# Kernel optimization log

Measured on AMD Instinct MI355X. Metric: run time of the kernel, lower is better.

Reference implementation:

```python
import jax, jax.numpy as jnp
import numpy as np

R = 32       # voxel_resolution
GROUPS = 8   # GroupNorm groups
EPS = 1e-5


def setup_inputs() -> dict:
    key = jax.random.key(0)
    ks = jax.random.split(key, 8)
    B, N, Cin, Cout = 4, 16384, 64, 128
    coords = jax.random.uniform(ks[0], (B, N, 3), dtype=jnp.float32)
    features = jax.random.normal(ks[1], (B, Cin, N), dtype=jnp.float32) * 0.5
    s1 = 1.0 / np.sqrt(Cin * 27)
    s2 = 1.0 / np.sqrt(Cout * 27)
    sm = 1.0 / np.sqrt(Cin)
    return {
        "coords": coords,
        "features": features,
        "conv1_w": jax.random.normal(ks[2], (Cout, Cin, 3, 3, 3), dtype=jnp.float32) * s1,
        "conv1_b": jnp.zeros((Cout,), jnp.float32),
        "gn1_g": jnp.ones((Cout,), jnp.float32),
        "gn1_b": jnp.zeros((Cout,), jnp.float32),
        "conv2_w": jax.random.normal(ks[3], (Cout, Cout, 3, 3, 3), dtype=jnp.float32) * s2,
        "conv2_b": jnp.zeros((Cout,), jnp.float32),
        "gn2_g": jnp.ones((Cout,), jnp.float32),
        "gn2_b": jnp.zeros((Cout,), jnp.float32),
        "mlp_w": jax.random.normal(ks[4], (Cout, Cin), dtype=jnp.float32) * sm,
        "mlp_b": jnp.zeros((Cout,), jnp.float32),
        "gnp_g": jnp.ones((Cout,), jnp.float32),
        "gnp_b": jnp.zeros((Cout,), jnp.float32),
    }


def _group_norm(x, gamma, beta, axes):
    # x: [B, C, ...]; normalize within channel groups over `axes` of the
    # grouped view [B, G, C//G, ...]. axes=(2,) => per-location GN (matches
    # nn.GroupNorm applied to per-voxel feature rows [Nvox, C]).
    B, C = x.shape[0], x.shape[1]
    xr = x.reshape(B, GROUPS, C // GROUPS, *x.shape[2:])
    mu = xr.mean(axis=axes, keepdims=True)
    var = ((xr - mu) ** 2).mean(axis=axes, keepdims=True)
    xn = ((xr - mu) * jax.lax.rsqrt(var + EPS)).reshape(x.shape)
    shp = (1, C) + (1,) * (x.ndim - 2)
    return xn * gamma.reshape(shp) + beta.reshape(shp)


def _conv3(x, w, b):
    y = jax.lax.conv_general_dilated(
        x, w, (1, 1, 1), 'SAME',
        dimension_numbers=('NCDHW', 'OIDHW', 'NCDHW'))
    return y + b.reshape(1, -1, 1, 1, 1)


def reference(coords, features, conv1_w, conv1_b, gn1_g, gn1_b,
              conv2_w, conv2_b, gn2_g, gn2_b, mlp_w, mlp_b, gnp_g, gnp_b):
    B, Cin, N = features.shape
    Cout = conv1_w.shape[0]

    # ---- voxelize: average-scatter point features into [B,Cin,R,R,R] ----
    c = coords * R                               # voxel-unit coords in [0,R)
    lo = jnp.floor(c)
    idx = jnp.clip(lo.astype(jnp.int32), 0, R - 1)   # [B,N,3]
    bidx = jnp.arange(B, dtype=jnp.int32)[:, None]
    flat = ((bidx * R + idx[..., 0]) * R + idx[..., 1]) * R + idx[..., 2]
    seg = flat.reshape(-1)                       # [B*N]
    fT = features.transpose(0, 2, 1).reshape(B * N, Cin)
    sums = jax.ops.segment_sum(fT, seg, num_segments=B * R * R * R)
    cnt = jax.ops.segment_sum(jnp.ones((B * N,), fT.dtype), seg,
                              num_segments=B * R * R * R)
    grid = (sums / jnp.maximum(cnt, 1.0)[:, None]).reshape(
        B, R, R, R, Cin).transpose(0, 4, 1, 2, 3)

    # ---- voxel branch: conv -> GN -> SiLU -> (dropout=id) -> conv -> GN -> SiLU
    h = jax.nn.silu(_group_norm(_conv3(grid, conv1_w, conv1_b), gn1_g, gn1_b, (2,)))
    h = jax.nn.silu(_group_norm(_conv3(h, conv2_w, conv2_b), gn2_g, gn2_b, (2,)))

    # ---- trilinear devoxelize: gather-interpolate back to points ----
    frac = c - lo                                # [B,N,3]
    hi = jnp.clip(idx + 1, 0, R - 1)
    gridf = h.transpose(0, 2, 3, 4, 1).reshape(B, R * R * R, Cout)
    barange = jnp.arange(B)[:, None]
    out = jnp.zeros((B, N, Cout), h.dtype)
    for dx in (0, 1):
        wx = frac[..., 0] if dx else 1.0 - frac[..., 0]
        ix = hi[..., 0] if dx else idx[..., 0]
        for dy in (0, 1):
            wy = frac[..., 1] if dy else 1.0 - frac[..., 1]
            iy = hi[..., 1] if dy else idx[..., 1]
            for dz in (0, 1):
                wz = frac[..., 2] if dz else 1.0 - frac[..., 2]
                iz = hi[..., 2] if dz else idx[..., 2]
                fi = (ix * R + iy) * R + iz       # [B,N]
                vals = gridf[barange, fi]         # [B,N,Cout]
                out = out + (wx * wy * wz)[..., None] * vals
    vox_pts = out.transpose(0, 2, 1)              # [B,Cout,N]

    # ---- point branch: SharedMLP = 1x1 conv + GroupNorm + SiLU ----
    pf = jnp.einsum('oi,bin->bon', mlp_w, features) + mlp_b[None, :, None]
    pf = jax.nn.silu(_group_norm(pf, gnp_g, gnp_b, (2, 3)))

    return pf + vox_pts
```

## Files before the change

kernel.cpp:

```cpp
#include <hip/hip_runtime.h>

typedef unsigned short u16;
typedef __attribute__((ext_vector_type(8))) short s16x8;
typedef __attribute__((ext_vector_type(4))) float f32x4;

#define R3 32768
#define NPTS 16384

__device__ __forceinline__ float b2f(u16 u) {
  union { unsigned int i; float f; } v; v.i = ((unsigned int)u) << 16; return v.f;
}
__device__ __forceinline__ u16 f2b(float f) {
  union { float f; unsigned int i; } v; v.f = f;
  unsigned int x = v.i;
  return (u16)((x + 0x7fffu + ((x >> 16) & 1u)) >> 16);
}
__device__ __forceinline__ void split2(float x, u16& h, u16& l) {
  h = f2b(x); l = f2b(x - b2f(h));
}
__device__ __forceinline__ float silu(float x) {
  return x / (1.f + __expf(-x));
}

__global__ void convert_weights(const float* __restrict__ w1, const float* __restrict__ w2,
                                const float* __restrict__ wm,
                                u16* __restrict__ Wh1, u16* __restrict__ Wl1,
                                u16* __restrict__ Wh2, u16* __restrict__ Wl2,
                                u16* __restrict__ Whm, u16* __restrict__ Wlm) {
  int e = blockIdx.x * 256 + threadIdx.x;
  if (e < 27 * 128 * 64) {
    int t = e / (128 * 64), co = (e / 64) % 128, ci = e % 64;
    split2(w1[(co * 64 + ci) * 27 + t], Wh1[e], Wl1[e]);
  }
  if (e < 27 * 128 * 128) {
    int t = e / (128 * 128), co = (e / 128) % 128, ci = e % 128;
    split2(w2[(co * 128 + ci) * 27 + t], Wh2[e], Wl2[e]);
  }
  if (e < 128 * 64) split2(wm[e], Whm[e], Wlm[e]);
}

__global__ void calc_pvox(const float* __restrict__ coords, int* __restrict__ pvox) {
  int t = blockIdx.x * 256 + threadIdx.x;
  if (t >= 4 * NPTS) return;
  const float* cp = coords + (size_t)t * 3;
  int ix = min(max((int)floorf(cp[0] * 32.f), 0), 31);
  int iy = min(max((int)floorf(cp[1] * 32.f), 0), 31);
  int iz = min(max((int)floorf(cp[2] * 32.f), 0), 31);
  pvox[t] = (ix * 32 + iy) * 32 + iz;
}

__global__ void __launch_bounds__(256)
scatter_feats(const float* __restrict__ features, const int* __restrict__ pvox,
              float* __restrict__ Gsum, float* __restrict__ Gcnt) {
  __shared__ float trans[64][65];
  __shared__ int vox[64];
  const int tid = threadIdx.x;
  const int bi = blockIdx.x >> 8;
  const int n0 = (blockIdx.x & 255) << 6;
  if (tid < 64) vox[tid] = pvox[bi * NPTS + n0 + tid];
  for (int e = tid; e < 4096; e += 256) {
    int ci = e >> 6, nn = e & 63;
    trans[nn][ci] = features[((size_t)bi * 64 + ci) * NPTS + n0 + nn];
  }
  __syncthreads();
  const int wave = tid >> 6, lane = tid & 63;
  for (int pi = 0; pi < 16; ++pi) {
    int nn = wave * 16 + pi;
    int v = vox[nn];
    atomicAdd(&Gsum[((size_t)bi * R3 + v) * 64 + lane], trans[nn][lane]);
    if (lane == 0) atomicAdd(&Gcnt[bi * R3 + v], 1.f);
  }
}

__global__ void __launch_bounds__(256)
finalize_grid(const float* __restrict__ Gsum, const float* __restrict__ Gcnt,
              u16* __restrict__ X1) {
  size_t g = (size_t)blockIdx.x * 256 + threadIdx.x;
  float c = fmaxf(Gcnt[g >> 4], 1.f);
  float4 s = ((const float4*)Gsum)[g];
  unsigned h0 = f2b(s.x / c), h1 = f2b(s.y / c), h2 = f2b(s.z / c), h3 = f2b(s.w / c);
  uint2 o; o.x = h0 | (h1 << 16); o.y = h2 | (h3 << 16);
  *(uint2*)(X1 + g * 4) = o;
}

template<int CIN>
__global__ void __launch_bounds__(256)
conv_mfma16(const u16* __restrict__ X, const u16* __restrict__ Wh, const u16* __restrict__ Wl,
            const float* __restrict__ bias, const float* __restrict__ gamma,
            const float* __restrict__ beta, u16* __restrict__ Yb) {
  constexpr int CINP = CIN + 8;
  constexpr int ROWS = 136;
  constexpr int KS = CIN / 32;
  constexpr int XBYTES = ROWS * CINP * 2;
  constexpr int SBYTES = 4 * 2 * 32 * 33 * 4;
  __shared__ __align__(16) char ldsbuf[(XBYTES > SBYTES) ? XBYTES : SBYTES];
  u16* Xs = (u16*)ldsbuf;
  float* ldsW = (float*)ldsbuf;

  const int tid = threadIdx.x;
  const int wave = tid >> 6, lane = tid & 63;
  const int l15 = lane & 15, q = lane >> 4;
  const int cobase = wave * 32;

  const int bi = blockIdx.x >> 8;
  const int rem = blockIdx.x & 255;
  const int x = rem >> 3, y0 = (rem & 7) << 2;

  u16 oneb = f2b(1.0f), lidb = f2b((float)(l15 + 1));
  s16x8 vone, vlid;
#pragma unroll
  for (int e = 0; e < 8; ++e) { vone[e] = (short)oneb; vlid[e] = (short)lidb; }
  f32x4 z4 = {0.f, 0.f, 0.f, 0.f};
  f32x4 d1 = __builtin_amdgcn_mfma_f32_16x16x32_bf16(vlid, vone, z4, 0, 0, 0);
  f32x4 d2 = __builtin_amdgcn_mfma_f32_16x16x32_bf16(vone, vlid, z4, 0, 0, 0);
  int mdec[4], ndec[4];
#pragma unroll
  for (int r = 0; r < 4; ++r) {
    mdec[r] = (int)(d1[r] * 0.03125f + 0.5f) - 1;
    ndec[r] = (int)(d2[r] * 0.03125f + 0.5f) - 1;
  }

  f32x4 acc[2][2][4];
#pragma unroll
  for (int a = 0; a < 2; ++a)
#pragma unroll
    for (int b = 0; b < 2; ++b)
#pragma unroll
      for (int c = 0; c < 4; ++c) acc[a][b][c] = (f32x4){0.f, 0.f, 0.f, 0.f};

  constexpr int CH8 = CIN / 8;
  for (int g = 0; g < 9; ++g) {
    __syncthreads();
    const int dx = g / 3 - 1, dy = g % 3 - 1;
    const int xs = x + dx;
    for (int c = tid; c < ROWS * CH8; c += 256) {
      int rr = c / CH8, k = (c % CH8) * 8;
      uint4 val; val.x = val.y = val.z = val.w = 0u;
      int vy = rr / 34;
      int zz = rr - vy * 34 - 1;
      int ys = y0 + vy + dy;
      if (xs >= 0 && xs < 32 && ys >= 0 && ys < 32 && zz >= 0 && zz < 32)
        val = *(const uint4*)(X + ((size_t)bi * R3 + (size_t)((xs * 32 + ys) * 32 + zz)) * CIN + k);
      *(uint4*)(&Xs[rr * CINP + k]) = val;
    }
    __syncthreads();
    for (int dz = 0; dz < 3; ++dz) {
      const int t = g * 3 + dz;
#pragma unroll
      for (int kb = 0; kb < KS; ++kb) {
        const int ko = kb * 32 + q * 8;
        s16x8 ah[2], al[2], bb[2][4];
#pragma unroll
        for (int ct = 0; ct < 2; ++ct) {
          size_t wo = ((size_t)(t * 128 + cobase + ct * 16 + l15)) * CIN + ko;
          ah[ct] = *(const s16x8*)(Wh + wo);
          al[ct] = *(const s16x8*)(Wl + wo);
        }
#pragma unroll
        for (int vt = 0; vt < 2; ++vt)
#pragma unroll
          for (int ln = 0; ln < 4; ++ln)
            bb[vt][ln] = *(const s16x8*)(&Xs[(ln * 34 + vt * 16 + l15 + dz) * CINP + ko]);
#pragma unroll
        for (int ct = 0; ct < 2; ++ct)
#pragma unroll
          for (int vt = 0; vt < 2; ++vt)
#pragma unroll
            for (int ln = 0; ln < 4; ++ln) {
              acc[ct][vt][ln] = __builtin_amdgcn_mfma_f32_16x16x32_bf16(
                  ah[ct], bb[vt][ln], acc[ct][vt][ln], 0, 0, 0);
              acc[ct][vt][ln] = __builtin_amdgcn_mfma_f32_16x16x32_bf16(
                  al[ct], bb[vt][ln], acc[ct][vt][ln], 0, 0, 0);
            }
      }
    }
  }

  const int half = lane >> 5, zl = lane & 31;
  for (int p = 0; p < 2; ++p) {
    __syncthreads();
#pragma unroll
    for (int l2 = 0; l2 < 2; ++l2)
#pragma unroll
      for (int ct = 0; ct < 2; ++ct)
#pragma unroll
        for (int vt = 0; vt < 2; ++vt)
#pragma unroll
          for (int r = 0; r < 4; ++r)
            ldsW[((wave * 2 + l2) * 32 + ct * 16 + mdec[r]) * 33 + vt * 16 + ndec[r]] =
                acc[ct][vt][2 * p + l2][r];
    __syncthreads();
    const int co0 = cobase + half * 16;
#pragma unroll
    for (int l2 = 0; l2 < 2; ++l2) {
      float v[16];
#pragma unroll
      for (int j = 0; j < 16; ++j)
        v[j] = ldsW[((wave * 2 + l2) * 32 + half * 16 + j) * 33 + zl] + bias[co0 + j];
      float mu = 0.f;
#pragma unroll
      for (int j = 0; j < 16; ++j) mu += v[j];
      mu *= 0.0625f;
      float var = 0.f;
#pragma unroll
      for (int j = 0; j < 16; ++j) { float d = v[j] - mu; var = fmaf(d, d, var); }
      var *= 0.0625f;
      float rs = rsqrtf(var + 1e-5f);
#pragma unroll
      for (int j = 0; j < 16; ++j) {
        float xn = (v[j] - mu) * rs * gamma[co0 + j] + beta[co0 + j];
        v[j] = silu(xn);
      }
      size_t row = (size_t)bi * R3 + (size_t)((x * 32 + y0 + 2 * p + l2) * 32 + zl);
      u16 outv[16];
#pragma unroll
      for (int j = 0; j < 16; ++j) outv[j] = f2b(v[j]);
      u16* yp = Yb + row * 128 + co0;
      *(uint4*)(yp)     = *(uint4*)(outv);
      *(uint4*)(yp + 8) = *(uint4*)(outv + 8);
    }
  }
}

__global__ void __launch_bounds__(256)
mlp_mfma(const float* __restrict__ features, const u16* __restrict__ Whm,
         const u16* __restrict__ Wlm, const float* __restrict__ mb,
         u16* __restrict__ pf, float* __restrict__ stats) {
  constexpr int XBYTES = 64 * 72 * 2;
  constexpr int SBYTES = 4 * 64 * 33 * 4;
  __shared__ __align__(16) char ldsbuf[(XBYTES > SBYTES) ? XBYTES : SBYTES];
  u16* Xs = (u16*)ldsbuf;
  float* ldsW = (float*)ldsbuf;

  const int tid = threadIdx.x;
  const int wave = tid >> 6, lane = tid & 63;
  const int l15 = lane & 15, q = lane >> 4;
  const int cobase = wave * 32;
  const int bi = blockIdx.x >> 8;
  const int n0 = (blockIdx.x & 255) << 6;

  u16 oneb = f2b(1.0f), lidb = f2b((float)(l15 + 1));
  s16x8 vone, vlid;
#pragma unroll
  for (int e = 0; e < 8; ++e) { vone[e] = (short)oneb; vlid[e] = (short)lidb; }
  f32x4 z4 = {0.f, 0.f, 0.f, 0.f};
  f32x4 d1 = __builtin_amdgcn_mfma_f32_16x16x32_bf16(vlid, vone, z4, 0, 0, 0);
  f32x4 d2 = __builtin_amdgcn_mfma_f32_16x16x32_bf16(vone, vlid, z4, 0, 0, 0);
  int mdec[4], ndec[4];
#pragma unroll
  for (int r = 0; r < 4; ++r) {
    mdec[r] = (int)(d1[r] * 0.03125f + 0.5f) - 1;
    ndec[r] = (int)(d2[r] * 0.03125f + 0.5f) - 1;
  }

  for (int e = tid; e < 4096; e += 256) {
    int ci = e >> 6, nn = e & 63;
    Xs[nn * 72 + ci] = f2b(features[((size_t)bi * 64 + ci) * NPTS + n0 + nn]);
  }
  __syncthreads();

  f32x4 acc[2][4];
#pragma unroll
  for (int a = 0; a < 2; ++a)
#pragma unroll
    for (int b = 0; b < 4; ++b) acc[a][b] = (f32x4){0.f, 0.f, 0.f, 0.f};

#pragma unroll
  for (int kb = 0; kb < 2; ++kb) {
    const int ko = kb * 32 + q * 8;
    s16x8 ah[2], al[2], bb[4];
#pragma unroll
    for (int ct = 0; ct < 2; ++ct) {
      size_t wo = ((size_t)(cobase + ct * 16 + l15)) * 64 + ko;
      ah[ct] = *(const s16x8*)(Whm + wo);
      al[ct] = *(const s16x8*)(Wlm + wo);
    }
#pragma unroll
    for (int vt = 0; vt < 4; ++vt)
      bb[vt] = *(const s16x8*)(&Xs[(vt * 16 + l15) * 72 + ko]);
#pragma unroll
    for (int ct = 0; ct < 2; ++ct)
#pragma unroll
      for (int vt = 0; vt < 4; ++vt) {
        acc[ct][vt] = __builtin_amdgcn_mfma_f32_16x16x32_bf16(ah[ct], bb[vt], acc[ct][vt], 0, 0, 0);
        acc[ct][vt] = __builtin_amdgcn_mfma_f32_16x16x32_bf16(al[ct], bb[vt], acc[ct][vt], 0, 0, 0);
      }
  }

  __syncthreads();
#pragma unroll
  for (int ct = 0; ct < 2; ++ct)
#pragma unroll
    for (int vt = 0; vt < 4; ++vt)
#pragma unroll
      for (int r = 0; r < 4; ++r)
        ldsW[(wave * 64 + vt * 16 + ndec[r]) * 33 + ct * 16 + mdec[r]] = acc[ct][vt][r];
  __syncthreads();

  float v[32];
  float s0 = 0.f, q0 = 0.f, s1 = 0.f, q1 = 0.f;
#pragma unroll
  for (int j = 0; j < 32; ++j) {
    v[j] = ldsW[(wave * 64 + lane) * 33 + j] + mb[cobase + j];
    if (j < 16) { s0 += v[j]; q0 = fmaf(v[j], v[j], q0); }
    else        { s1 += v[j]; q1 = fmaf(v[j], v[j], q1); }
  }
  u16 outv[32];
#pragma unroll
  for (int j = 0; j < 32; ++j) outv[j] = f2b(v[j]);
  u16* yp = pf + ((size_t)bi * NPTS + n0 + lane) * 128 + cobase;
#pragma unroll
  for (int k = 0; k < 4; ++k) *(uint4*)(yp + 8 * k) = *(uint4*)(outv + 8 * k);

#pragma unroll
  for (int off = 32; off > 0; off >>= 1) {
    s0 += __shfl_xor(s0, off); q0 += __shfl_xor(q0, off);
    s1 += __shfl_xor(s1, off); q1 += __shfl_xor(q1, off);
  }
  if (lane == 0) {
    atomicAdd(&stats[(bi * 8 + 2 * wave + 0) * 2 + 0], s0);
    atomicAdd(&stats[(bi * 8 + 2 * wave + 0) * 2 + 1], q0);
    atomicAdd(&stats[(bi * 8 + 2 * wave + 1) * 2 + 0], s1);
    atomicAdd(&stats[(bi * 8 + 2 * wave + 1) * 2 + 1], q1);
  }
}

__global__ void __launch_bounds__(256)
final_fuse(const float* __restrict__ coords, const u16* __restrict__ H,
           const u16* __restrict__ pf, const float* __restrict__ stats,
           const float* __restrict__ gg, const float* __restrict__ gb,
           float* __restrict__ out) {
  __shared__ float trans[64][130];
  const int tid = threadIdx.x;
  const int wave = tid >> 6, lane = tid & 63;
  const int bi = blockIdx.x >> 8;
  const int p0 = (blockIdx.x & 255) << 6;
  const int co = lane * 2;
  const int grp = co >> 4;
  const float cntInv = 1.f / (16.f * 16384.f);
  float S  = stats[(bi * 8 + grp) * 2 + 0];
  float SS = stats[(bi * 8 + grp) * 2 + 1];
  float mu = S * cntInv;
  float var = SS * cntInv - mu * mu;
  float rs = rsqrtf(var + 1e-5f);
  float g0 = gg[co], g1 = gg[co + 1], b0 = gb[co], b1 = gb[co + 1];

  for (int pi = 0; pi < 16; ++pi) {
    int pl = wave * 16 + pi;
    int p = p0 + pl;
    const float* cp = coords + ((size_t)bi * NPTS + p) * 3;
    float cx = cp[0] * 32.f, cy = cp[1] * 32.f, cz = cp[2] * 32.f;
    float fx = floorf(cx), fy = floorf(cy), fz = floorf(cz);
    int ix = min(max((int)fx, 0), 31);
    int iy = min(max((int)fy, 0), 31);
    int iz = min(max((int)fz, 0), 31);
    float rx = cx - fx, ry = cy - fy, rz = cz - fz;
    int hx = min(ix + 1, 31), hy = min(iy + 1, 31), hz = min(iz + 1, 31);
    float a0 = 0.f, a1 = 0.f;
#pragma unroll
    for (int k = 0; k < 8; ++k) {
      int xb = k >> 2, yb = (k >> 1) & 1, zb = k & 1;
      float w = (xb ? rx : 1.f - rx) * (yb ? ry : 1.f - ry) * (zb ? rz : 1.f - rz);
      int vi = ((xb ? hx : ix) * 32 + (yb ? hy : iy)) * 32 + (zb ? hz : iz);
      unsigned hv = *(const unsigned*)(H + ((size_t)bi * R3 + vi) * 128 + co);
      a0 += w * b2f((u16)(hv & 0xffff));
      a1 += w * b2f((u16)(hv >> 16));
    }
    unsigned pv = *(const unsigned*)(pf + ((size_t)bi * NPTS + p) * 128 + co);
    float q0 = (b2f((u16)(pv & 0xffff)) - mu) * rs * g0 + b0;
    float q1 = (b2f((u16)(pv >> 16)) - mu) * rs * g1 + b1;
    trans[pl][co]     = silu(q0) + a0;
    trans[pl][co + 1] = silu(q1) + a1;
  }
  __syncthreads();
  for (int e = tid; e < 8192; e += 256) {
    int c = e >> 6, pp = e & 63;
    out[((size_t)bi * 128 + c) * NPTS + p0 + pp] = trans[pp][c];
  }
}

extern "C" void kernel_launch(void* const* d_in, const int* in_sizes, int n_in,
                              void* d_out, int out_size, void* d_ws, size_t ws_size,
                              hipStream_t stream) {
  const float* coords   = (const float*)d_in[0];
  const float* features = (const float*)d_in[1];
  const float* conv1_w  = (const float*)d_in[2];
  const float* conv1_b  = (const float*)d_in[3];
  const float* gn1_g    = (const float*)d_in[4];
  const float* gn1_b    = (const float*)d_in[5];
  const float* conv2_w  = (const float*)d_in[6];
  const float* conv2_b  = (const float*)d_in[7];
  const float* gn2_g    = (const float*)d_in[8];
  const float* gn2_b    = (const float*)d_in[9];
  const float* mlp_w    = (const float*)d_in[10];
  const float* mlp_b    = (const float*)d_in[11];
  const float* gnp_g    = (const float*)d_in[12];
  const float* gnp_b    = (const float*)d_in[13];

  char* ws = (char*)d_ws;
  float* Gsum = (float*)(ws + 0);
  u16*   H    = (u16*)(ws + 0);
  u16*   X1   = (u16*)(ws + 33554432);
  u16*   X2   = (u16*)(ws + 50331648);
  float* Gcnt = (float*)(ws + 83886080);
  float* stats = (float*)(ws + 84410368);
  int*   pvox = (int*)(ws + 84414464);
  u16*   pf   = (u16*)(ws + 84676608);
  u16*   Wh1  = (u16*)(ws + 101453824);
  u16*   Wl1  = (u16*)(ws + 101896192);
  u16*   Wh2  = (u16*)(ws + 102338560);
  u16*   Wl2  = (u16*)(ws + 103223296);
  u16*   Whm  = (u16*)(ws + 104108032);
  u16*   Wlm  = (u16*)(ws + 104124416);

  hipMemsetAsync(ws, 0, 33554432, stream);
  hipMemsetAsync(ws + 83886080, 0, 524288 + 4096, stream);

  convert_weights<<<(27 * 128 * 128 + 255) / 256, 256, 0, stream>>>(
      conv1_w, conv2_w, mlp_w, Wh1, Wl1, Wh2, Wl2, Whm, Wlm);
  calc_pvox<<<(4 * NPTS + 255) / 256, 256, 0, stream>>>(coords, pvox);
  scatter_feats<<<1024, 256, 0, stream>>>(features, pvox, Gsum, Gcnt);
  finalize_grid<<<8192, 256, 0, stream>>>(Gsum, Gcnt, X1);
  conv_mfma16<64><<<1024, 256, 0, stream>>>(
      X1, Wh1, Wl1, conv1_b, gn1_g, gn1_b, X2);
  mlp_mfma<<<1024, 256, 0, stream>>>(features, Whm, Wlm, mlp_b, pf, stats);
  conv_mfma16<128><<<1024, 256, 0, stream>>>(
      X2, Wh2, Wl2, conv2_b, gn2_g, gn2_b, H);
  final_fuse<<<1024, 256, 0, stream>>>(coords, H, pf, stats, gnp_g, gnp_b,
                                       (float*)d_out);
}
```

Baseline: 647.5 us.

## Split conv output channels across two blocks with XCD-aware tile mapping

Each conv block now computes 64 output channels instead of 128, with each wave doing a single 16-channel tile. This doubles the grid to 2048 blocks and cuts accumulator registers, and launch bounds now ask for 4 blocks per SM. Block IDs are remapped so the tiles on each XCD share spatial neighbourhoods, which should improve L2 reuse. The cost is that every input halo tile is loaded into LDS twice, once per channel half, so global and LDS load traffic per MFMA goes up.

```diff
diff --git a/kernel.cpp b/kernel.cpp
--- a/kernel.cpp
+++ b/kernel.cpp
@@ -84,15 +84,16 @@
 }
 
 template<int CIN>
-__global__ void __launch_bounds__(256)
-conv_mfma16(const u16* __restrict__ X, const u16* __restrict__ Wh, const u16* __restrict__ Wl,
-            const float* __restrict__ bias, const float* __restrict__ gamma,
-            const float* __restrict__ beta, u16* __restrict__ Yb) {
+__global__ void __launch_bounds__(256, 4)
+conv_mfma16c(const u16* __restrict__ X, const u16* __restrict__ Wh, const u16* __restrict__ Wl,
+             const float* __restrict__ bias, const float* __restrict__ gamma,
+             const float* __restrict__ beta, u16* __restrict__ Yb) {
   constexpr int CINP = CIN + 8;
   constexpr int ROWS = 136;
   constexpr int KS = CIN / 32;
+  constexpr int CH8 = CIN / 8;
   constexpr int XBYTES = ROWS * CINP * 2;
-  constexpr int SBYTES = 4 * 2 * 32 * 33 * 4;
+  constexpr int SBYTES = 4 * 2 * 16 * 33 * 4;
   __shared__ __align__(16) char ldsbuf[(XBYTES > SBYTES) ? XBYTES : SBYTES];
   u16* Xs = (u16*)ldsbuf;
   float* ldsW = (float*)ldsbuf;
@@ -100,11 +101,15 @@
   const int tid = threadIdx.x;
   const int wave = tid >> 6, lane = tid & 63;
   const int l15 = lane & 15, q = lane >> 4;
-  const int cobase = wave * 32;
-
-  const int bi = blockIdx.x >> 8;
-  const int rem = blockIdx.x & 255;
+
+  const int bid = blockIdx.x;
+  const int xcd = bid & 7, jj = bid >> 3;
+  const int coblk = jj >> 7;
+  const int tile = xcd * 128 + (jj & 127);
+  const int bi = tile >> 8;
+  const int rem = tile & 255;
   const int x = rem >> 3, y0 = (rem & 7) << 2;
+  const int co0 = coblk * 64 + wave * 16;
 
   u16 oneb = f2b(1.0f), lidb = f2b((float)(l15 + 1));
   s16x8 vone, vlid;
@@ -120,15 +125,12 @@
     ndec[r] = (int)(d2[r] * 0.03125f + 0.5f) - 1;
   }
 
-  f32x4 acc[2][2][4];
-#pragma unroll
-  for (int a = 0; a < 2; ++a)
-#pragma unroll
-    for (int b = 0; b < 2; ++b)
-#pragma unroll
-      for (int c = 0; c < 4; ++c) acc[a][b][c] = (f32x4){0.f, 0.f, 0.f, 0.f};
-
-  constexpr int CH8 = CIN / 8;
+  f32x4 acc[2][4];
+#pragma unroll
+  for (int b = 0; b < 2; ++b)
+#pragma unroll
+    for (int c = 0; c < 4; ++c) acc[b][c] = (f32x4){0.f, 0.f, 0.f, 0.f};
+
   for (int g = 0; g < 9; ++g) {
     __syncthreads();
     const int dx = g / 3 - 1, dy = g % 3 - 1;
@@ -149,12 +151,11 @@
 #pragma unroll
       for (int kb = 0; kb < KS; ++kb) {
         const int ko = kb * 32 + q * 8;
-        s16x8 ah[2], al[2], bb[2][4];
-#pragma unroll
-        for (int ct = 0; ct < 2; ++ct) {
-          size_t wo = ((size_t)(t * 128 + cobase + ct * 16 + l15)) * CIN + ko;
-          ah[ct] = *(const s16x8*)(Wh + wo);
-          al[ct] = *(const s16x8*)(Wl + wo);
+        s16x8 ah, al, bb[2][4];
+        {
+          size_t wo = ((size_t)(t * 128 + co0 + l15)) * CIN + ko;
+          ah = *(const s16x8*)(Wh + wo);
+          al = *(const s16x8*)(Wl + wo);
         }
 #pragma unroll
         for (int vt = 0; vt < 2; ++vt)
@@ -162,16 +163,14 @@
           for (int ln = 0; ln < 4; ++ln)
             bb[vt][ln] = *(const s16x8*)(&Xs[(ln * 34 + vt * 16 + l15 + dz) * CINP + ko]);
 #pragma unroll
-        for (int ct = 0; ct < 2; ++ct)
-#pragma unroll
-          for (int vt = 0; vt < 2; ++vt)
-#pragma unroll
-            for (int ln = 0; ln < 4; ++ln) {
-              acc[ct][vt][ln] = __builtin_amdgcn_mfma_f32_16x16x32_bf16(
-                  ah[ct], bb[vt][ln], acc[ct][vt][ln], 0, 0, 0);
-              acc[ct][vt][ln] = __builtin_amdgcn_mfma_f32_16x16x32_bf16(
-                  al[ct], bb[vt][ln], acc[ct][vt][ln], 0, 0, 0);
-            }
+        for (int vt = 0; vt < 2; ++vt)
+#pragma unroll
+          for (int ln = 0; ln < 4; ++ln) {
+            acc[vt][ln] = __builtin_amdgcn_mfma_f32_16x16x32_bf16(
+                ah, bb[vt][ln], acc[vt][ln], 0, 0, 0);
+            acc[vt][ln] = __builtin_amdgcn_mfma_f32_16x16x32_bf16(
+                al, bb[vt][ln], acc[vt][ln], 0, 0, 0);
+          }
       }
     }
   }
@@ -182,43 +181,37 @@
 #pragma unroll
     for (int l2 = 0; l2 < 2; ++l2)
 #pragma unroll
-      for (int ct = 0; ct < 2; ++ct)
-#pragma unroll
-        for (int vt = 0; vt < 2; ++vt)
-#pragma unroll
-          for (int r = 0; r < 4; ++r)
-            ldsW[((wave * 2 + l2) * 32 + ct * 16 + mdec[r]) * 33 + vt * 16 + ndec[r]] =
-                acc[ct][vt][2 * p + l2][r];
+      for (int vt = 0; vt < 2; ++vt)
+#pragma unroll
+        for (int r = 0; r < 4; ++r)
+          ldsW[((wave * 2 + l2) * 16 + mdec[r]) * 33 + vt * 16 + ndec[r]] =
+              acc[vt][2 * p + l2][r];
     __syncthreads();
-    const int co0 = cobase + half * 16;
-#pragma unroll
-    for (int l2 = 0; l2 < 2; ++l2) {
-      float v[16];
-#pragma unroll
-      for (int j = 0; j < 16; ++j)
-        v[j] = ldsW[((wave * 2 + l2) * 32 + half * 16 + j) * 33 + zl] + bias[co0 + j];
-      float mu = 0.f;
-#pragma unroll
-      for (int j = 0; j < 16; ++j) mu += v[j];
-      mu *= 0.0625f;
-      float var = 0.f;
-#pragma unroll
-      for (int j = 0; j < 16; ++j) { float d = v[j] - mu; var = fmaf(d, d, var); }
-      var *= 0.0625f;
-      float rs = rsqrtf(var + 1e-5f);
-#pragma unroll
-      for (int j = 0; j < 16; ++j) {
-        float xn = (v[j] - mu) * rs * gamma[co0 + j] + beta[co0 + j];
-        v[j] = silu(xn);
-      }
-      size_t row = (size_t)bi * R3 + (size_t)((x * 32 + y0 + 2 * p + l2) * 32 + zl);
-      u16 outv[16];
-#pragma unroll
-      for (int j = 0; j < 16; ++j) outv[j] = f2b(v[j]);
-      u16* yp = Yb + row * 128 + co0;
-      *(uint4*)(yp)     = *(uint4*)(outv);
-      *(uint4*)(yp + 8) = *(uint4*)(outv + 8);
+    float v[16];
+#pragma unroll
+    for (int j = 0; j < 16; ++j)
+      v[j] = ldsW[((wave * 2 + half) * 16 + j) * 33 + zl] + bias[co0 + j];
+    float mu = 0.f;
+#pragma unroll
+    for (int j = 0; j < 16; ++j) mu += v[j];
+    mu *= 0.0625f;
+    float var = 0.f;
+#pragma unroll
+    for (int j = 0; j < 16; ++j) { float d = v[j] - mu; var = fmaf(d, d, var); }
+    var *= 0.0625f;
+    float rs = rsqrtf(var + 1e-5f);
+#pragma unroll
+    for (int j = 0; j < 16; ++j) {
+      float xn = (v[j] - mu) * rs * gamma[co0 + j] + beta[co0 + j];
+      v[j] = silu(xn);
     }
+    size_t row = (size_t)bi * R3 + (size_t)((x * 32 + y0 + 2 * p + half) * 32 + zl);
+    u16 outv[16];
+#pragma unroll
+    for (int j = 0; j < 16; ++j) outv[j] = f2b(v[j]);
+    u16* yp = Yb + row * 128 + co0;
+    *(uint4*)(yp)     = *(uint4*)(outv);
+    *(uint4*)(yp + 8) = *(uint4*)(outv + 8);
   }
 }
 
@@ -421,10 +414,10 @@
   calc_pvox<<<(4 * NPTS + 255) / 256, 256, 0, stream>>>(coords, pvox);
   scatter_feats<<<1024, 256, 0, stream>>>(features, pvox, Gsum, Gcnt);
   finalize_grid<<<8192, 256, 0, stream>>>(Gsum, Gcnt, X1);
-  conv_mfma16<64><<<1024, 256, 0, stream>>>(
+  conv_mfma16c<64><<<2048, 256, 0, stream>>>(
       X1, Wh1, Wl1, conv1_b, gn1_g, gn1_b, X2);
   mlp_mfma<<<1024, 256, 0, stream>>>(features, Whm, Wlm, mlp_b, pf, stats);
-  conv_mfma16<128><<<1024, 256, 0, stream>>>(
+  conv_mfma16c<128><<<2048, 256, 0, stream>>>(
       X2, Wh2, Wl2, conv2_b, gn2_g, gn2_b, H);
   final_fuse<<<1024, 256, 0, stream>>>(coords, H, pf, stats, gnp_g, gnp_b,
                                        (float*)d_out);
```

After: 664.7 us. +2.6%, slower.

## Re-split conv waves over channels and y-lines; fuse voxel index into scatter

Applied to the files above, without the earlier changes.

The conv kernel now assigns each wave 64 output channels and 2 y-lines instead of 32 channels and 4 lines. This trades fewer LDS activation loads per wave for more global weight loads. The GroupNorm/SiLU epilogue is reorganised so each thread handles 32 channels of one voxel. The separate voxel-index kernel is folded into the scatter kernel to remove a launch and a buffer round trip.

```diff
diff --git a/kernel.cpp b/kernel.cpp
--- a/kernel.cpp
+++ b/kernel.cpp
@@ -39,25 +39,21 @@
   if (e < 128 * 64) split2(wm[e], Whm[e], Wlm[e]);
 }
 
-__global__ void calc_pvox(const float* __restrict__ coords, int* __restrict__ pvox) {
-  int t = blockIdx.x * 256 + threadIdx.x;
-  if (t >= 4 * NPTS) return;
-  const float* cp = coords + (size_t)t * 3;
-  int ix = min(max((int)floorf(cp[0] * 32.f), 0), 31);
-  int iy = min(max((int)floorf(cp[1] * 32.f), 0), 31);
-  int iz = min(max((int)floorf(cp[2] * 32.f), 0), 31);
-  pvox[t] = (ix * 32 + iy) * 32 + iz;
-}
-
 __global__ void __launch_bounds__(256)
-scatter_feats(const float* __restrict__ features, const int* __restrict__ pvox,
+scatter_feats(const float* __restrict__ coords, const float* __restrict__ features,
               float* __restrict__ Gsum, float* __restrict__ Gcnt) {
   __shared__ float trans[64][65];
   __shared__ int vox[64];
   const int tid = threadIdx.x;
   const int bi = blockIdx.x >> 8;
   const int n0 = (blockIdx.x & 255) << 6;
-  if (tid < 64) vox[tid] = pvox[bi * NPTS + n0 + tid];
+  if (tid < 64) {
+    const float* cp = coords + ((size_t)bi * NPTS + n0 + tid) * 3;
+    int ix = min(max((int)floorf(cp[0] * 32.f), 0), 31);
+    int iy = min(max((int)floorf(cp[1] * 32.f), 0), 31);
+    int iz = min(max((int)floorf(cp[2] * 32.f), 0), 31);
+    vox[tid] = (ix * 32 + iy) * 32 + iz;
+  }
   for (int e = tid; e < 4096; e += 256) {
     int ci = e >> 6, nn = e & 63;
     trans[nn][ci] = features[((size_t)bi * 64 + ci) * NPTS + n0 + nn];
@@ -85,14 +81,15 @@
 
 template<int CIN>
 __global__ void __launch_bounds__(256)
-conv_mfma16(const u16* __restrict__ X, const u16* __restrict__ Wh, const u16* __restrict__ Wl,
-            const float* __restrict__ bias, const float* __restrict__ gamma,
-            const float* __restrict__ beta, u16* __restrict__ Yb) {
+conv_mfma_c4(const u16* __restrict__ X, const u16* __restrict__ Wh, const u16* __restrict__ Wl,
+             const float* __restrict__ bias, const float* __restrict__ gamma,
+             const float* __restrict__ beta, u16* __restrict__ Yb) {
   constexpr int CINP = CIN + 8;
   constexpr int ROWS = 136;
   constexpr int KS = CIN / 32;
+  constexpr int CH8 = CIN / 8;
   constexpr int XBYTES = ROWS * CINP * 2;
-  constexpr int SBYTES = 4 * 2 * 32 * 33 * 4;
+  constexpr int SBYTES = 2 * 128 * 33 * 4;
   __shared__ __align__(16) char ldsbuf[(XBYTES > SBYTES) ? XBYTES : SBYTES];
   u16* Xs = (u16*)ldsbuf;
   float* ldsW = (float*)ldsbuf;
@@ -100,7 +97,8 @@
   const int tid = threadIdx.x;
   const int wave = tid >> 6, lane = tid & 63;
   const int l15 = lane & 15, q = lane >> 4;
-  const int cobase = wave * 32;
+  const int cohalf = wave & 1, yhalf = wave >> 1;
+  const int co0 = cohalf * 64;
 
   const int bi = blockIdx.x >> 8;
   const int rem = blockIdx.x & 255;
@@ -120,15 +118,14 @@
     ndec[r] = (int)(d2[r] * 0.03125f + 0.5f) - 1;
   }
 
-  f32x4 acc[2][2][4];
-#pragma unroll
-  for (int a = 0; a < 2; ++a)
+  f32x4 acc[4][2][2];
+#pragma unroll
+  for (int a = 0; a < 4; ++a)
 #pragma unroll
     for (int b = 0; b < 2; ++b)
 #pragma unroll
-      for (int c = 0; c < 4; ++c) acc[a][b][c] = (f32x4){0.f, 0.f, 0.f, 0.f};
-
-  constexpr int CH8 = CIN / 8;
+      for (int c = 0; c < 2; ++c) acc[a][b][c] = (f32x4){0.f, 0.f, 0.f, 0.f};
+
   for (int g = 0; g < 9; ++g) {
     __syncthreads();
     const int dx = g / 3 - 1, dy = g % 3 - 1;
@@ -149,76 +146,77 @@
 #pragma unroll
       for (int kb = 0; kb < KS; ++kb) {
         const int ko = kb * 32 + q * 8;
-        s16x8 ah[2], al[2], bb[2][4];
-#pragma unroll
-        for (int ct = 0; ct < 2; ++ct) {
-          size_t wo = ((size_t)(t * 128 + cobase + ct * 16 + l15)) * CIN + ko;
+        s16x8 ah[4], al[4], bb[2][2];
+#pragma unroll
+        for (int ct = 0; ct < 4; ++ct) {
+          size_t wo = ((size_t)(t * 128 + co0 + ct * 16 + l15)) * CIN + ko;
           ah[ct] = *(const s16x8*)(Wh + wo);
           al[ct] = *(const s16x8*)(Wl + wo);
         }
 #pragma unroll
-        for (int vt = 0; vt < 2; ++vt)
-#pragma unroll
-          for (int ln = 0; ln < 4; ++ln)
-            bb[vt][ln] = *(const s16x8*)(&Xs[(ln * 34 + vt * 16 + l15 + dz) * CINP + ko]);
-#pragma unroll
-        for (int ct = 0; ct < 2; ++ct)
+        for (int l2 = 0; l2 < 2; ++l2)
 #pragma unroll
           for (int vt = 0; vt < 2; ++vt)
-#pragma unroll
-            for (int ln = 0; ln < 4; ++ln) {
-              acc[ct][vt][ln] = __builtin_amdgcn_mfma_f32_16x16x32_bf16(
-                  ah[ct], bb[vt][ln], acc[ct][vt][ln], 0, 0, 0);
-              acc[ct][vt][ln] = __builtin_amdgcn_mfma_f32_16x16x32_bf16(
-                  al[ct], bb[vt][ln], acc[ct][vt][ln], 0, 0, 0);
+            bb[l2][vt] = *(const s16x8*)(
+                &Xs[((yhalf * 2 + l2) * 34 + vt * 16 + l15 + dz) * CINP + ko]);
+#pragma unroll
+        for (int ct = 0; ct < 4; ++ct)
+#pragma unroll
+          for (int vt = 0; vt < 2; ++vt)
+#pragma unroll
+            for (int l2 = 0; l2 < 2; ++l2) {
+              acc[ct][vt][l2] = __builtin_amdgcn_mfma_f32_16x16x32_bf16(
+                  ah[ct], bb[l2][vt], acc[ct][vt][l2], 0, 0, 0);
+              acc[ct][vt][l2] = __builtin_amdgcn_mfma_f32_16x16x32_bf16(
+                  al[ct], bb[l2][vt], acc[ct][vt][l2], 0, 0, 0);
             }
       }
     }
   }
 
-  const int half = lane >> 5, zl = lane & 31;
   for (int p = 0; p < 2; ++p) {
     __syncthreads();
 #pragma unroll
-    for (int l2 = 0; l2 < 2; ++l2)
-#pragma unroll
-      for (int ct = 0; ct < 2; ++ct)
-#pragma unroll
-        for (int vt = 0; vt < 2; ++vt)
-#pragma unroll
-          for (int r = 0; r < 4; ++r)
-            ldsW[((wave * 2 + l2) * 32 + ct * 16 + mdec[r]) * 33 + vt * 16 + ndec[r]] =
-                acc[ct][vt][2 * p + l2][r];
+    for (int ct = 0; ct < 4; ++ct)
+#pragma unroll
+      for (int vt = 0; vt < 2; ++vt)
+#pragma unroll
+        for (int r = 0; r < 4; ++r) {
+          int co = co0 + ct * 16 + mdec[r];
+          int z  = vt * 16 + ndec[r];
+          ldsW[(yhalf * 128 + co) * 33 + z] = acc[ct][vt][p][r];
+        }
     __syncthreads();
-    const int co0 = cobase + half * 16;
-#pragma unroll
-    for (int l2 = 0; l2 < 2; ++l2) {
-      float v[16];
-#pragma unroll
-      for (int j = 0; j < 16; ++j)
-        v[j] = ldsW[((wave * 2 + l2) * 32 + half * 16 + j) * 33 + zl] + bias[co0 + j];
-      float mu = 0.f;
-#pragma unroll
-      for (int j = 0; j < 16; ++j) mu += v[j];
-      mu *= 0.0625f;
-      float var = 0.f;
-#pragma unroll
-      for (int j = 0; j < 16; ++j) { float d = v[j] - mu; var = fmaf(d, d, var); }
-      var *= 0.0625f;
-      float rs = rsqrtf(var + 1e-5f);
-#pragma unroll
-      for (int j = 0; j < 16; ++j) {
-        float xn = (v[j] - mu) * rs * gamma[co0 + j] + beta[co0 + j];
-        v[j] = silu(xn);
-      }
-      size_t row = (size_t)bi * R3 + (size_t)((x * 32 + y0 + 2 * p + l2) * 32 + zl);
-      u16 outv[16];
-#pragma unroll
-      for (int j = 0; j < 16; ++j) outv[j] = f2b(v[j]);
-      u16* yp = Yb + row * 128 + co0;
-      *(uint4*)(yp)     = *(uint4*)(outv);
-      *(uint4*)(yp + 8) = *(uint4*)(outv + 8);
-    }
+    const int vx = tid >> 2, quarter = tid & 3;
+    const int lsel = vx >> 5, z = vx & 31;
+    const int cq = quarter * 32;
+    float v[32];
+#pragma unroll
+    for (int j = 0; j < 32; ++j)
+      v[j] = ldsW[(lsel * 128 + cq + j) * 33 + z] + bias[cq + j];
+    float mu0 = 0.f, mu1 = 0.f;
+#pragma unroll
+    for (int j = 0; j < 16; ++j) { mu0 += v[j]; mu1 += v[16 + j]; }
+    mu0 *= 0.0625f; mu1 *= 0.0625f;
+    float va0 = 0.f, va1 = 0.f;
+#pragma unroll
+    for (int j = 0; j < 16; ++j) {
+      float d0 = v[j] - mu0;      va0 = fmaf(d0, d0, va0);
+      float d1v = v[16 + j] - mu1; va1 = fmaf(d1v, d1v, va1);
+    }
+    float rs0 = rsqrtf(va0 * 0.0625f + 1e-5f);
+    float rs1 = rsqrtf(va1 * 0.0625f + 1e-5f);
+    u16 outv[32];
+#pragma unroll
+    for (int j = 0; j < 32; ++j) {
+      float mu = (j < 16) ? mu0 : mu1, rs = (j < 16) ? rs0 : rs1;
+      float xn = (v[j] - mu) * rs * gamma[cq + j] + beta[cq + j];
+      outv[j] = f2b(silu(xn));
+    }
+    size_t row = (size_t)bi * R3 + (size_t)((x * 32 + y0 + lsel * 2 + p) * 32 + z);
+    u16* yp = Yb + row * 128 + cq;
+#pragma unroll
+    for (int k = 0; k < 4; ++k) *(uint4*)(yp + 8 * k) = *(uint4*)(outv + 8 * k);
   }
 }
 
@@ -404,7 +402,6 @@
   u16*   X2   = (u16*)(ws + 50331648);
   float* Gcnt = (float*)(ws + 83886080);
   float* stats = (float*)(ws + 84410368);
-  int*   pvox = (int*)(ws + 84414464);
   u16*   pf   = (u16*)(ws + 84676608);
   u16*   Wh1  = (u16*)(ws + 101453824);
   u16*   Wl1  = (u16*)(ws + 101896192);
@@ -418,13 +415,12 @@
 
   convert_weights<<<(27 * 128 * 128 + 255) / 256, 256, 0, stream>>>(
       conv1_w, conv2_w, mlp_w, Wh1, Wl1, Wh2, Wl2, Whm, Wlm);
-  calc_pvox<<<(4 * NPTS + 255) / 256, 256, 0, stream>>>(coords, pvox);
-  scatter_feats<<<1024, 256, 0, stream>>>(features, pvox, Gsum, Gcnt);
+  scatter_feats<<<1024, 256, 0, stream>>>(coords, features, Gsum, Gcnt);
   finalize_grid<<<8192, 256, 0, stream>>>(Gsum, Gcnt, X1);
-  conv_mfma16<64><<<1024, 256, 0, stream>>>(
+  conv_mfma_c4<64><<<1024, 256, 0, stream>>>(
       X1, Wh1, Wl1, conv1_b, gn1_g, gn1_b, X2);
   mlp_mfma<<<1024, 256, 0, stream>>>(features, Whm, Wlm, mlp_b, pf, stats);
-  conv_mfma16<128><<<1024, 256, 0, stream>>>(
+  conv_mfma_c4<128><<<1024, 256, 0, stream>>>(
       X2, Wh2, Wl2, conv2_b, gn2_g, gn2_b, H);
   final_fuse<<<1024, 256, 0, stream>>>(coords, H, pf, stats, gnp_g, gnp_b,
                                        (float*)d_out);
```

Measured after the change: 945.4 us. +46.0%, slower.

## Stage 6-row y halo per x-slice in conv and fuse voxel index into scatter

Applied to the files above, without the earlier changes.

The conv kernels now load one LDS tile per x offset, holding six y rows (ROWS 204) with the z halo, and reuse it across all three dy and three dz taps. Before, a fresh four-row tile was loaded for each of nine (dx,dy) pairs, so this cuts global loads and block barriers from nine to three per block. The cost is more LDS per block (about 55 KB for CIN=128), which may lower occupancy. The separate calc_pvox kernel is also removed and its voxel index computation is folded into scatter_feats, saving one launch and an intermediate buffer.

```diff
diff --git a/kernel.cpp b/kernel.cpp
--- a/kernel.cpp
+++ b/kernel.cpp
@@ -39,25 +39,21 @@
   if (e < 128 * 64) split2(wm[e], Whm[e], Wlm[e]);
 }
 
-__global__ void calc_pvox(const float* __restrict__ coords, int* __restrict__ pvox) {
-  int t = blockIdx.x * 256 + threadIdx.x;
-  if (t >= 4 * NPTS) return;
-  const float* cp = coords + (size_t)t * 3;
-  int ix = min(max((int)floorf(cp[0] * 32.f), 0), 31);
-  int iy = min(max((int)floorf(cp[1] * 32.f), 0), 31);
-  int iz = min(max((int)floorf(cp[2] * 32.f), 0), 31);
-  pvox[t] = (ix * 32 + iy) * 32 + iz;
-}
-
 __global__ void __launch_bounds__(256)
-scatter_feats(const float* __restrict__ features, const int* __restrict__ pvox,
+scatter_feats(const float* __restrict__ coords, const float* __restrict__ features,
               float* __restrict__ Gsum, float* __restrict__ Gcnt) {
   __shared__ float trans[64][65];
   __shared__ int vox[64];
   const int tid = threadIdx.x;
   const int bi = blockIdx.x >> 8;
   const int n0 = (blockIdx.x & 255) << 6;
-  if (tid < 64) vox[tid] = pvox[bi * NPTS + n0 + tid];
+  if (tid < 64) {
+    const float* cp = coords + ((size_t)bi * NPTS + n0 + tid) * 3;
+    int ix = min(max((int)floorf(cp[0] * 32.f), 0), 31);
+    int iy = min(max((int)floorf(cp[1] * 32.f), 0), 31);
+    int iz = min(max((int)floorf(cp[2] * 32.f), 0), 31);
+    vox[tid] = (ix * 32 + iy) * 32 + iz;
+  }
   for (int e = tid; e < 4096; e += 256) {
     int ci = e >> 6, nn = e & 63;
     trans[nn][ci] = features[((size_t)bi * 64 + ci) * NPTS + n0 + nn];
@@ -85,12 +81,14 @@
 
 template<int CIN>
 __global__ void __launch_bounds__(256)
-conv_mfma16(const u16* __restrict__ X, const u16* __restrict__ Wh, const u16* __restrict__ Wl,
-            const float* __restrict__ bias, const float* __restrict__ gamma,
-            const float* __restrict__ beta, u16* __restrict__ Yb) {
+conv_mfma_s3(const u16* __restrict__ X, const u16* __restrict__ Wh, const u16* __restrict__ Wl,
+             const float* __restrict__ bias, const float* __restrict__ gamma,
+             const float* __restrict__ beta, u16* __restrict__ Yb) {
   constexpr int CINP = CIN + 8;
-  constexpr int ROWS = 136;
+  constexpr int ROWS = 204;
+  constexpr int CH8 = CIN / 8;
   constexpr int KS = CIN / 32;
+  constexpr int NCH = ROWS * CH8;
   constexpr int XBYTES = ROWS * CINP * 2;
   constexpr int SBYTES = 4 * 2 * 32 * 33 * 4;
   __shared__ __align__(16) char ldsbuf[(XBYTES > SBYTES) ? XBYTES : SBYTES];
@@ -128,50 +126,54 @@
 #pragma unroll
       for (int c = 0; c < 4; ++c) acc[a][b][c] = (f32x4){0.f, 0.f, 0.f, 0.f};
 
-  constexpr int CH8 = CIN / 8;
-  for (int g = 0; g < 9; ++g) {
+  for (int dxs = 0; dxs < 3; ++dxs) {
     __syncthreads();
-    const int dx = g / 3 - 1, dy = g % 3 - 1;
-    const int xs = x + dx;
-    for (int c = tid; c < ROWS * CH8; c += 256) {
+    const int xs = x + dxs - 1;
+    for (int c = tid; c < NCH; c += 256) {
       int rr = c / CH8, k = (c % CH8) * 8;
       uint4 val; val.x = val.y = val.z = val.w = 0u;
-      int vy = rr / 34;
-      int zz = rr - vy * 34 - 1;
-      int ys = y0 + vy + dy;
+      int jy = rr / 34;
+      int pz = rr - jy * 34;
+      int ys = y0 + jy - 1, zz = pz - 1;
       if (xs >= 0 && xs < 32 && ys >= 0 && ys < 32 && zz >= 0 && zz < 32)
         val = *(const uint4*)(X + ((size_t)bi * R3 + (size_t)((xs * 32 + ys) * 32 + zz)) * CIN + k);
       *(uint4*)(&Xs[rr * CINP + k]) = val;
     }
     __syncthreads();
-    for (int dz = 0; dz < 3; ++dz) {
-      const int t = g * 3 + dz;
-#pragma unroll
-      for (int kb = 0; kb < KS; ++kb) {
-        const int ko = kb * 32 + q * 8;
-        s16x8 ah[2], al[2], bb[2][4];
-#pragma unroll
-        for (int ct = 0; ct < 2; ++ct) {
-          size_t wo = ((size_t)(t * 128 + cobase + ct * 16 + l15)) * CIN + ko;
-          ah[ct] = *(const s16x8*)(Wh + wo);
-          al[ct] = *(const s16x8*)(Wl + wo);
+    for (int dy = 0; dy < 3; ++dy) {
+      const int tb = dxs * 9 + dy * 3;
+      const int rbase = dy * 34;
+#pragma unroll
+      for (int dz = 0; dz < 3; ++dz) {
+        const int t = tb + dz;
+#pragma unroll
+        for (int kb = 0; kb < KS; ++kb) {
+          const int ko = kb * 32 + q * 8;
+          s16x8 ah[2], al[2], bb[2][4];
+#pragma unroll
+          for (int ct = 0; ct < 2; ++ct) {
+            size_t wo = ((size_t)(t * 128 + cobase + ct * 16 + l15)) * CIN + ko;
+            ah[ct] = *(const s16x8*)(Wh + wo);
+            al[ct] = *(const s16x8*)(Wl + wo);
+          }
+#pragma unroll
+          for (int vt = 0; vt < 2; ++vt)
+#pragma unroll
+            for (int ln = 0; ln < 4; ++ln)
+              bb[vt][ln] = *(const s16x8*)(
+                  &Xs[(rbase + ln * 34 + vt * 16 + l15 + dz) * CINP + ko]);
+#pragma unroll
+          for (int ct = 0; ct < 2; ++ct)
+#pragma unroll
+            for (int vt = 0; vt < 2; ++vt)
+#pragma unroll
+              for (int ln = 0; ln < 4; ++ln) {
+                acc[ct][vt][ln] = __builtin_amdgcn_mfma_f32_16x16x32_bf16(
+                    ah[ct], bb[vt][ln], acc[ct][vt][ln], 0, 0, 0);
+                acc[ct][vt][ln] = __builtin_amdgcn_mfma_f32_16x16x32_bf16(
+                    al[ct], bb[vt][ln], acc[ct][vt][ln], 0, 0, 0);
+              }
         }
-#pragma unroll
-        for (int vt = 0; vt < 2; ++vt)
-#pragma unroll
-          for (int ln = 0; ln < 4; ++ln)
-            bb[vt][ln] = *(const s16x8*)(&Xs[(ln * 34 + vt * 16 + l15 + dz) * CINP + ko]);
-#pragma unroll
-        for (int ct = 0; ct < 2; ++ct)
-#pragma unroll
-          for (int vt = 0; vt < 2; ++vt)
-#pragma unroll
-            for (int ln = 0; ln < 4; ++ln) {
-              acc[ct][vt][ln] = __builtin_amdgcn_mfma_f32_16x16x32_bf16(
-                  ah[ct], bb[vt][ln], acc[ct][vt][ln], 0, 0, 0);
-              acc[ct][vt][ln] = __builtin_amdgcn_mfma_f32_16x16x32_bf16(
-                  al[ct], bb[vt][ln], acc[ct][vt][ln], 0, 0, 0);
-            }
       }
     }
   }
@@ -404,7 +406,6 @@
   u16*   X2   = (u16*)(ws + 50331648);
   float* Gcnt = (float*)(ws + 83886080);
   float* stats = (float*)(ws + 84410368);
-  int*   pvox = (int*)(ws + 84414464);
   u16*   pf   = (u16*)(ws + 84676608);
   u16*   Wh1  = (u16*)(ws + 101453824);
   u16*   Wl1  = (u16*)(ws + 101896192);
@@ -418,13 +419,12 @@
 
   convert_weights<<<(27 * 128 * 128 + 255) / 256, 256, 0, stream>>>(
       conv1_w, conv2_w, mlp_w, Wh1, Wl1, Wh2, Wl2, Whm, Wlm);
-  calc_pvox<<<(4 * NPTS + 255) / 256, 256, 0, stream>>>(coords, pvox);
-  scatter_feats<<<1024, 256, 0, stream>>>(features, pvox, Gsum, Gcnt);
+  scatter_feats<<<1024, 256, 0, stream>>>(coords, features, Gsum, Gcnt);
   finalize_grid<<<8192, 256, 0, stream>>>(Gsum, Gcnt, X1);
-  conv_mfma16<64><<<1024, 256, 0, stream>>>(
+  conv_mfma_s3<64><<<1024, 256, 0, stream>>>(
       X1, Wh1, Wl1, conv1_b, gn1_g, gn1_b, X2);
   mlp_mfma<<<1024, 256, 0, stream>>>(features, Whm, Wlm, mlp_b, pf, stats);
-  conv_mfma16<128><<<1024, 256, 0, stream>>>(
+  conv_mfma_s3<128><<<1024, 256, 0, stream>>>(
       X2, Wh2, Wl2, conv2_b, gn2_g, gn2_b, H);
   final_fuse<<<1024, 256, 0, stream>>>(coords, H, pf, stats, gnp_g, gnp_b,
                                        (float*)d_out);
```

After: 641.3 us. No clear change (-1.0%).
